# Kernel optimization log

Measured on AMD Instinct MI355X. Metric: run time of the kernel, lower is better.

Reference implementation:

```python
import jax, jax.numpy as jnp
import numpy as np

NUM_GRAPHS = 64
MAX_NODES = 512
D_MODEL = 512


def _lengths():
    # deterministic variable graph sizes in [256, 512]
    return 256 + (np.arange(NUM_GRAPHS) * 7) % 257


def setup_inputs() -> dict:
    key = jax.random.key(0)
    lengths = _lengths()
    total = int(lengths.sum())  # 23557
    # per-node graph id and within-graph position (replaces torch.split + pad_sequence)
    graph_ids = np.repeat(np.arange(NUM_GRAPHS, dtype=np.int32), lengths)
    pos_ids = np.concatenate([np.arange(n, dtype=np.int32) for n in lengths])
    batched_h = jax.random.normal(key, (total, D_MODEL), dtype=jnp.float32)
    return {
        "batched_h": batched_h,
        "graph_ids": jnp.asarray(graph_ids),
        "pos_ids": jnp.asarray(pos_ids),
        "B": NUM_GRAPHS,
        "max_n": MAX_NODES,
    }


def reference(batched_h, graph_ids, pos_ids, B, max_n):
    # pad_sequence equivalent: scatter nodes into [B, max_n, D] zero-padded tensor
    D = batched_h.shape[-1]
    padded = jnp.zeros((B, max_n, D), dtype=batched_h.dtype)
    padded = padded.at[graph_ids, pos_ids].set(batched_h)
    # Wq = Wk = Identity; bmm(q, k^T) -> [B, max_n, max_n]
    inst_out = jnp.einsum("bnd,bmd->bnm", padded, padded)
    # return_feat=False -> feat_out is empty; return inst_out only
    return inst_out
```

## Files before the change

### kernel.cpp

```cpp
#include <hip/hip_runtime.h>
#include <hip/hip_bf16.h>

#define DCONST 512
#define MAXN   512
#define NGRAPH 64

typedef __bf16 bf16x8 __attribute__((ext_vector_type(8)));
typedef float  f32x4  __attribute__((ext_vector_type(4)));
typedef float  fvec4  __attribute__((ext_vector_type(4)));

__global__ void pad_convert(const float* __restrict__ h,
                            __bf16* __restrict__ padded)
{
    const int t   = blockIdx.x * blockDim.x + threadIdx.x;
    const int row = t >> 6;
    const int seg = t & 63;
    const int g   = row >> 9;
    const int p   = row & 511;

    int off = 0, m7 = 0;
    for (int i = 0; i < g; ++i) {
        off += 256 + m7;
        m7 += 7; if (m7 >= 257) m7 -= 257;
    }
    const int len = 256 + m7;

    bf16x8 v = {};
    if (p < len) {
        const fvec4* src = reinterpret_cast<const fvec4*>(
            h + (size_t)(off + p) * DCONST + seg * 8);
        fvec4 a = src[0];
        fvec4 b = src[1];
        v[0] = (__bf16)a[0]; v[1] = (__bf16)a[1]; v[2] = (__bf16)a[2]; v[3] = (__bf16)a[3];
        v[4] = (__bf16)b[0]; v[5] = (__bf16)b[1]; v[6] = (__bf16)b[2]; v[7] = (__bf16)b[3];
    }
    *reinterpret_cast<bf16x8*>(padded + (size_t)row * DCONST + seg * 8) = v;
}

__constant__ const int TI10[10] = {0,0,0,0,1,1,1,2,2,3};
__constant__ const int TJ10[10] = {0,1,2,3,1,2,3,2,3,3};

__global__ __launch_bounds__(256, 3) void gemm_xxt(const __bf16* __restrict__ X,
                                                   float* __restrict__ out)
{
    __shared__ __align__(16) __bf16 ldsA[3][128][32];
    __shared__ __align__(16) __bf16 ldsB[3][128][32];

    const int bid = blockIdx.x;
    const int xcd = bid & 7;
    const int idx = bid >> 3;
    const int g   = xcd * 8 + idx / 10;
    const int tl  = idx % 10;
    const int ti  = TI10[tl];
    const int tj  = TJ10[tl];
    const bool diag = (ti == tj);
    const int row0 = ti * 128;
    const int col0 = tj * 128;

    const __bf16* __restrict__ Xg = X + (size_t)g * MAXN * DCONST;

    const int tid  = threadIdx.x;
    const int wave = tid >> 6;
    const int lane = tid & 63;
    const int wr   = wave >> 1;
    const int wc   = wave & 1;

    const int lrow  = lane >> 2;
    const int lslot = lane & 3;

    auto stage = [&](int s) {
        const int buf = s % 3;
        const int k0  = s * 32;
        #pragma unroll
        for (int r = 0; r < 2; ++r) {
            const int rbase = r * 64 + wave * 16;
            const int row   = rbase + lrow;
            const int chunk = lslot ^ ((row >> 1) & 3);
            const __bf16* gA = Xg + (size_t)(row0 + row) * DCONST + k0 + chunk * 8;
            __builtin_amdgcn_global_load_lds(gA, &ldsA[buf][rbase][0], 16, 0, 0);
            const int rB = diag ? row0 + row : col0 + row;
            const __bf16* gB = Xg + (size_t)rB * DCONST + k0 + chunk * 8;
            __builtin_amdgcn_global_load_lds(gB, &ldsB[buf][rbase][0], 16, 0, 0);
        }
    };

    stage(0);
    stage(1);
    asm volatile("s_waitcnt vmcnt(4)\n\ts_barrier" ::: "memory");

    const int fr = lane & 15;
    const int q  = lane >> 4;
    f32x4 acc[4][4] = {};

    #pragma unroll
    for (int s = 0; s < 16; ++s) {
        if (s + 2 < 16) stage(s + 2);

        const int buf = s % 3;
        bf16x8 afr[4], bfr[4];
        #pragma unroll
        for (int m = 0; m < 4; ++m) {
            const int rr = wr * 64 + m * 16 + fr;
            const int sl = (q ^ ((rr >> 1) & 3)) * 8;
            afr[m] = *reinterpret_cast<const bf16x8*>(&ldsA[buf][rr][sl]);
        }
        #pragma unroll
        for (int n = 0; n < 4; ++n) {
            const int rr = wc * 64 + n * 16 + fr;
            const int sl = (q ^ ((rr >> 1) & 3)) * 8;
            bfr[n] = *reinterpret_cast<const bf16x8*>(&ldsB[buf][rr][sl]);
        }

        #pragma unroll
        for (int m = 0; m < 4; ++m)
            #pragma unroll
            for (int n = 0; n < 4; ++n)
                acc[m][n] = __builtin_amdgcn_mfma_f32_16x16x32_bf16(
                    afr[m], bfr[n], acc[m][n], 0, 0, 0);

        if (s < 15) {
            if (s + 2 < 16) {
                asm volatile("s_waitcnt vmcnt(4)\n\ts_barrier" ::: "memory");
            } else {
                asm volatile("s_waitcnt vmcnt(0)\n\ts_barrier" ::: "memory");
            }
        }
    }

    float* __restrict__ og = out + (size_t)g * MAXN * MAXN;
    const int rl0 = wr * 64 + q * 4;
    const int cl0 = wc * 64 + fr;
    #pragma unroll
    for (int m = 0; m < 4; ++m) {
        #pragma unroll
        for (int n = 0; n < 4; ++n) {
            f32x4 v = acc[m][n];
            float* p = og + (size_t)(row0 + rl0 + m * 16) * MAXN + col0 + cl0 + n * 16;
            #pragma unroll
            for (int r = 0; r < 4; ++r)
                p[(size_t)r * MAXN] = v[r];
            if (!diag) {
                float* pT = og + (size_t)(col0 + cl0 + n * 16) * MAXN
                               + row0 + rl0 + m * 16;
                *reinterpret_cast<f32x4*>(pT) = v;
            }
        }
    }
}

extern "C" void kernel_launch(void* const* d_in, const int* in_sizes, int n_in,
                              void* d_out, int out_size, void* d_ws, size_t ws_size,
                              hipStream_t stream)
{
    const float* h   = (const float*)d_in[0];
    __bf16* padded   = (__bf16*)d_ws;
    float*  out      = (float*)d_out;

    const int rows = NGRAPH * MAXN;
    pad_convert<<<rows * 64 / 256, 256, 0, stream>>>(h, padded);

    gemm_xxt<<<dim3(NGRAPH * 10), dim3(256), 0, stream>>>(padded, out);
}
```

Before: 129.5 us.

## Fuse pad/convert into Gram kernel with per-graph atomic flag barrier

```diff
diff --git a/kernel.cpp b/kernel.cpp
--- a/kernel.cpp
+++ b/kernel.cpp
@@ -9,39 +9,13 @@
 typedef float  f32x4  __attribute__((ext_vector_type(4)));
 typedef float  fvec4  __attribute__((ext_vector_type(4)));
 
-__global__ void pad_convert(const float* __restrict__ h,
-                            __bf16* __restrict__ padded)
-{
-    const int t   = blockIdx.x * blockDim.x + threadIdx.x;
-    const int row = t >> 6;
-    const int seg = t & 63;
-    const int g   = row >> 9;
-    const int p   = row & 511;
-
-    int off = 0, m7 = 0;
-    for (int i = 0; i < g; ++i) {
-        off += 256 + m7;
-        m7 += 7; if (m7 >= 257) m7 -= 257;
-    }
-    const int len = 256 + m7;
-
-    bf16x8 v = {};
-    if (p < len) {
-        const fvec4* src = reinterpret_cast<const fvec4*>(
-            h + (size_t)(off + p) * DCONST + seg * 8);
-        fvec4 a = src[0];
-        fvec4 b = src[1];
-        v[0] = (__bf16)a[0]; v[1] = (__bf16)a[1]; v[2] = (__bf16)a[2]; v[3] = (__bf16)a[3];
-        v[4] = (__bf16)b[0]; v[5] = (__bf16)b[1]; v[6] = (__bf16)b[2]; v[7] = (__bf16)b[3];
-    }
-    *reinterpret_cast<bf16x8*>(padded + (size_t)row * DCONST + seg * 8) = v;
-}
-
 __constant__ const int TI10[10] = {0,0,0,0,1,1,1,2,2,3};
 __constant__ const int TJ10[10] = {0,1,2,3,1,2,3,2,3,3};
 
-__global__ __launch_bounds__(256, 3) void gemm_xxt(const __bf16* __restrict__ X,
-                                                   float* __restrict__ out)
+__global__ __launch_bounds__(256, 3) void fused_pad_gram(const float* __restrict__ h,
+                                                         __bf16* __restrict__ padded,
+                                                         float* __restrict__ out,
+                                                         unsigned* __restrict__ flags)
 {
     __shared__ __align__(16) __bf16 ldsA[3][128][32];
     __shared__ __align__(16) __bf16 ldsB[3][128][32];
@@ -57,9 +31,53 @@
     const int row0 = ti * 128;
     const int col0 = tj * 128;
 
-    const __bf16* __restrict__ Xg = X + (size_t)g * MAXN * DCONST;
+    int off = 0, m7 = 0;
+    for (int i = 0; i < g; ++i) {
+        off += 256 + m7;
+        m7 += 7; if (m7 >= 257) m7 -= 257;
+    }
+    const int len = 256 + m7;
 
     const int tid  = threadIdx.x;
+    __bf16* __restrict__ pg = padded + (size_t)g * MAXN * DCONST;
+
+    {
+        const int rbeg = tl * 52;
+        const int rend = (rbeg + 52 < MAXN) ? rbeg + 52 : MAXN;
+        const int seg  = tid & 63;
+        for (int r0 = rbeg; r0 < rend; r0 += 4) {
+            const int row = r0 + (tid >> 6);
+            if (row < rend) {
+                bf16x8 v = {};
+                if (row < len) {
+                    const fvec4* src = reinterpret_cast<const fvec4*>(
+                        h + (size_t)(off + row) * DCONST + seg * 8);
+                    fvec4 a = src[0];
+                    fvec4 b = src[1];
+                    v[0] = (__bf16)a[0]; v[1] = (__bf16)a[1];
+                    v[2] = (__bf16)a[2]; v[3] = (__bf16)a[3];
+                    v[4] = (__bf16)b[0]; v[5] = (__bf16)b[1];
+                    v[6] = (__bf16)b[2]; v[7] = (__bf16)b[3];
+                }
+                *reinterpret_cast<bf16x8*>(pg + (size_t)row * DCONST + seg * 8) = v;
+            }
+        }
+    }
+    __threadfence();
+    __syncthreads();
+    if (tid == 0)
+        __hip_atomic_fetch_add(&flags[g], 1u, __ATOMIC_RELEASE,
+                               __HIP_MEMORY_SCOPE_AGENT);
+
+    if (tid == 0) {
+        int guard = 0;
+        while (__hip_atomic_load(&flags[g], __ATOMIC_ACQUIRE,
+                                 __HIP_MEMORY_SCOPE_AGENT) != 10u &&
+               ++guard < 200000)
+            __builtin_amdgcn_s_sleep(2);
+    }
+    __syncthreads();
+
     const int wave = tid >> 6;
     const int lane = tid & 63;
     const int wr   = wave >> 1;
@@ -76,10 +94,10 @@
             const int rbase = r * 64 + wave * 16;
             const int row   = rbase + lrow;
             const int chunk = lslot ^ ((row >> 1) & 3);
-            const __bf16* gA = Xg + (size_t)(row0 + row) * DCONST + k0 + chunk * 8;
+            const __bf16* gA = pg + (size_t)(row0 + row) * DCONST + k0 + chunk * 8;
             __builtin_amdgcn_global_load_lds(gA, &ldsA[buf][rbase][0], 16, 0, 0);
             const int rB = diag ? row0 + row : col0 + row;
-            const __bf16* gB = Xg + (size_t)rB * DCONST + k0 + chunk * 8;
+            const __bf16* gB = pg + (size_t)rB * DCONST + k0 + chunk * 8;
             __builtin_amdgcn_global_load_lds(gB, &ldsB[buf][rbase][0], 16, 0, 0);
         }
     };
@@ -154,10 +172,10 @@
 {
     const float* h   = (const float*)d_in[0];
     __bf16* padded   = (__bf16*)d_ws;
+    unsigned* flags  = (unsigned*)((char*)d_ws + (size_t)32 * 1024 * 1024);
     float*  out      = (float*)d_out;
 
-    const int rows = NGRAPH * MAXN;
-    pad_convert<<<rows * 64 / 256, 256, 0, stream>>>(h, padded);
+    hipMemsetAsync(flags, 0, NGRAPH * sizeof(unsigned), stream);
 
-    gemm_xxt<<<dim3(NGRAPH * 10), dim3(256), 0, stream>>>(padded, out);
+    fused_pad_gram<<<dim3(NGRAPH * 10), dim3(256), 0, stream>>>(h, padded, out, flags);
 }
```

New measurement: 287.4 us. +121.9%, slower.

## Fuse pad/convert into Gram GEMM, loading fp32 rows directly into LDS

Applied to the files above, without the earlier changes.

```diff
diff --git a/kernel.cpp b/kernel.cpp
--- a/kernel.cpp
+++ b/kernel.cpp
@@ -7,44 +7,15 @@
 
 typedef __bf16 bf16x8 __attribute__((ext_vector_type(8)));
 typedef float  f32x4  __attribute__((ext_vector_type(4)));
-typedef float  fvec4  __attribute__((ext_vector_type(4)));
-
-__global__ void pad_convert(const float* __restrict__ h,
-                            __bf16* __restrict__ padded)
-{
-    const int t   = blockIdx.x * blockDim.x + threadIdx.x;
-    const int row = t >> 6;
-    const int seg = t & 63;
-    const int g   = row >> 9;
-    const int p   = row & 511;
-
-    int off = 0, m7 = 0;
-    for (int i = 0; i < g; ++i) {
-        off += 256 + m7;
-        m7 += 7; if (m7 >= 257) m7 -= 257;
-    }
-    const int len = 256 + m7;
-
-    bf16x8 v = {};
-    if (p < len) {
-        const fvec4* src = reinterpret_cast<const fvec4*>(
-            h + (size_t)(off + p) * DCONST + seg * 8);
-        fvec4 a = src[0];
-        fvec4 b = src[1];
-        v[0] = (__bf16)a[0]; v[1] = (__bf16)a[1]; v[2] = (__bf16)a[2]; v[3] = (__bf16)a[3];
-        v[4] = (__bf16)b[0]; v[5] = (__bf16)b[1]; v[6] = (__bf16)b[2]; v[7] = (__bf16)b[3];
-    }
-    *reinterpret_cast<bf16x8*>(padded + (size_t)row * DCONST + seg * 8) = v;
-}
 
 __constant__ const int TI10[10] = {0,0,0,0,1,1,1,2,2,3};
 __constant__ const int TJ10[10] = {0,1,2,3,1,2,3,2,3,3};
 
-__global__ __launch_bounds__(256, 3) void gemm_xxt(const __bf16* __restrict__ X,
-                                                   float* __restrict__ out)
+__global__ __launch_bounds__(256, 2) void gram_direct(const float* __restrict__ h,
+                                                      float* __restrict__ out)
 {
-    __shared__ __align__(16) __bf16 ldsA[3][128][32];
-    __shared__ __align__(16) __bf16 ldsB[3][128][32];
+    __shared__ __align__(16) float ldsA[2][128][32];
+    __shared__ __align__(16) float ldsB[2][128][32];
 
     const int bid = blockIdx.x;
     const int xcd = bid & 7;
@@ -57,7 +28,12 @@
     const int row0 = ti * 128;
     const int col0 = tj * 128;
 
-    const __bf16* __restrict__ Xg = X + (size_t)g * MAXN * DCONST;
+    int off = 0, m7 = 0;
+    for (int i = 0; i < g; ++i) {
+        off += 256 + m7;
+        m7 += 7; if (m7 >= 257) m7 -= 257;
+    }
+    const int len = 256 + m7;
 
     const int tid  = threadIdx.x;
     const int wave = tid >> 6;
@@ -65,50 +41,66 @@
     const int wr   = wave >> 1;
     const int wc   = wave & 1;
 
-    const int lrow  = lane >> 2;
-    const int lslot = lane & 3;
-
     auto stage = [&](int s) {
-        const int buf = s % 3;
+        const int buf = s & 1;
         const int k0  = s * 32;
         #pragma unroll
-        for (int r = 0; r < 2; ++r) {
-            const int rbase = r * 64 + wave * 16;
-            const int row   = rbase + lrow;
-            const int chunk = lslot ^ ((row >> 1) & 3);
-            const __bf16* gA = Xg + (size_t)(row0 + row) * DCONST + k0 + chunk * 8;
+        for (int r = 0; r < 4; ++r) {
+            const int rbase = r * 32 + wave * 8;
+            const int row   = rbase + (lane >> 3);
+            const int chunk = (lane & 7) ^ (row & 7);
+            const int ra  = row0 + row;
+            const int rca = ra < len ? ra : len - 1;
+            const float* gA = h + (size_t)(off + rca) * DCONST + k0 + chunk * 4;
             __builtin_amdgcn_global_load_lds(gA, &ldsA[buf][rbase][0], 16, 0, 0);
-            const int rB = diag ? row0 + row : col0 + row;
-            const __bf16* gB = Xg + (size_t)rB * DCONST + k0 + chunk * 8;
-            __builtin_amdgcn_global_load_lds(gB, &ldsB[buf][rbase][0], 16, 0, 0);
+            if (!diag) {
+                const int rb  = col0 + row;
+                const int rcb = rb < len ? rb : len - 1;
+                const float* gB = h + (size_t)(off + rcb) * DCONST + k0 + chunk * 4;
+                __builtin_amdgcn_global_load_lds(gB, &ldsB[buf][rbase][0], 16, 0, 0);
+            }
         }
     };
 
     stage(0);
-    stage(1);
-    asm volatile("s_waitcnt vmcnt(4)\n\ts_barrier" ::: "memory");
+    asm volatile("s_waitcnt vmcnt(0)\n\ts_barrier" ::: "memory");
 
     const int fr = lane & 15;
     const int q  = lane >> 4;
     f32x4 acc[4][4] = {};
 
+    const float* baseB0 = diag ? &ldsA[0][0][0] : &ldsB[0][0][0];
+    const float* baseB1 = diag ? &ldsA[1][0][0] : &ldsB[1][0][0];
+
     #pragma unroll
     for (int s = 0; s < 16; ++s) {
-        if (s + 2 < 16) stage(s + 2);
+        if (s < 15) stage(s + 1);
 
-        const int buf = s % 3;
+        const int buf = s & 1;
+        const float* bb = buf ? baseB1 : baseB0;
+
         bf16x8 afr[4], bfr[4];
         #pragma unroll
         for (int m = 0; m < 4; ++m) {
-            const int rr = wr * 64 + m * 16 + fr;
-            const int sl = (q ^ ((rr >> 1) & 3)) * 8;
-            afr[m] = *reinterpret_cast<const bf16x8*>(&ldsA[buf][rr][sl]);
+            const int rr  = wr * 64 + m * 16 + fr;
+            const int sw  = rr & 7;
+            f32x4 lo = *reinterpret_cast<const f32x4*>(&ldsA[buf][rr][((2*q)   ^ sw) * 4]);
+            f32x4 hi = *reinterpret_cast<const f32x4*>(&ldsA[buf][rr][((2*q+1) ^ sw) * 4]);
+            bf16x8 a;
+            a[0] = (__bf16)lo[0]; a[1] = (__bf16)lo[1]; a[2] = (__bf16)lo[2]; a[3] = (__bf16)lo[3];
+            a[4] = (__bf16)hi[0]; a[5] = (__bf16)hi[1]; a[6] = (__bf16)hi[2]; a[7] = (__bf16)hi[3];
+            afr[m] = a;
         }
         #pragma unroll
         for (int n = 0; n < 4; ++n) {
-            const int rr = wc * 64 + n * 16 + fr;
-            const int sl = (q ^ ((rr >> 1) & 3)) * 8;
-            bfr[n] = *reinterpret_cast<const bf16x8*>(&ldsB[buf][rr][sl]);
+            const int rr  = wc * 64 + n * 16 + fr;
+            const int sw  = rr & 7;
+            f32x4 lo = *reinterpret_cast<const f32x4*>(&bb[(size_t)rr * 32 + ((2*q)   ^ sw) * 4]);
+            f32x4 hi = *reinterpret_cast<const f32x4*>(&bb[(size_t)rr * 32 + ((2*q+1) ^ sw) * 4]);
+            bf16x8 b;
+            b[0] = (__bf16)lo[0]; b[1] = (__bf16)lo[1]; b[2] = (__bf16)lo[2]; b[3] = (__bf16)lo[3];
+            b[4] = (__bf16)hi[0]; b[5] = (__bf16)hi[1]; b[6] = (__bf16)hi[2]; b[7] = (__bf16)hi[3];
+            bfr[n] = b;
         }
 
         #pragma unroll
@@ -119,11 +111,7 @@
                     afr[m], bfr[n], acc[m][n], 0, 0, 0);
 
         if (s < 15) {
-            if (s + 2 < 16) {
-                asm volatile("s_waitcnt vmcnt(4)\n\ts_barrier" ::: "memory");
-            } else {
-                asm volatile("s_waitcnt vmcnt(0)\n\ts_barrier" ::: "memory");
-            }
+            asm volatile("s_waitcnt vmcnt(0)\n\ts_barrier" ::: "memory");
         }
     }
 
@@ -135,14 +123,21 @@
         #pragma unroll
         for (int n = 0; n < 4; ++n) {
             f32x4 v = acc[m][n];
-            float* p = og + (size_t)(row0 + rl0 + m * 16) * MAXN + col0 + cl0 + n * 16;
+            const int gj  = col0 + cl0 + n * 16;
+            const bool jok = gj < len;
+            f32x4 vm;
+            #pragma unroll
+            for (int r = 0; r < 4; ++r) {
+                const int gi = row0 + rl0 + m * 16 + r;
+                vm[r] = (jok && gi < len) ? v[r] : 0.0f;
+            }
+            float* p = og + (size_t)(row0 + rl0 + m * 16) * MAXN + gj;
             #pragma unroll
             for (int r = 0; r < 4; ++r)
-                p[(size_t)r * MAXN] = v[r];
+                p[(size_t)r * MAXN] = vm[r];
             if (!diag) {
-                float* pT = og + (size_t)(col0 + cl0 + n * 16) * MAXN
-                               + row0 + rl0 + m * 16;
-                *reinterpret_cast<f32x4*>(pT) = v;
+                float* pT = og + (size_t)gj * MAXN + row0 + rl0 + m * 16;
+                *reinterpret_cast<f32x4*>(pT) = vm;
             }
         }
     }
@@ -152,12 +147,9 @@
                               void* d_out, int out_size, void* d_ws, size_t ws_size,
                               hipStream_t stream)
 {
-    const float* h   = (const float*)d_in[0];
-    __bf16* padded   = (__bf16*)d_ws;
-    float*  out      = (float*)d_out;
+    const float* h = (const float*)d_in[0];
+    float* out     = (float*)d_out;
+    (void)d_ws; (void)ws_size;
 
-    const int rows = NGRAPH * MAXN;
-    pad_convert<<<rows * 64 / 256, 256, 0, stream>>>(h, padded);
-
-    gemm_xxt<<<dim3(NGRAPH * 10), dim3(256), 0, stream>>>(padded, out);
+    gram_direct<<<dim3(NGRAPH * 10), dim3(256), 0, stream>>>(h, out);
 }
```

Result: slower. 139.4 us (+7.6%).
